# Kernel optimization log

Measured on AMD Instinct MI355X. Metric: run time of the kernel, lower is better.

## Reference

```python
import jax, jax.numpy as jnp
import numpy as np

C = 1024
H = 16
K = 2  # num_states
B, N = 4, 4096


def setup_inputs() -> dict:
    key = jax.random.key(0)
    ks_ = jax.random.split(key, 12)
    s = 1.0 / np.sqrt(C)
    inp = {
        "x": jax.random.normal(ks_[0], (B, N, C), dtype=jnp.float32),
        "Wq": jax.random.normal(ks_[1], (C, C), dtype=jnp.float32) * s,
        "bq": jnp.zeros((C,), dtype=jnp.float32),
        "Wk": jax.random.normal(ks_[2], (K, C, C), dtype=jnp.float32) * s,
        "bk": jnp.zeros((K, C), dtype=jnp.float32),
        "Wv": jax.random.normal(ks_[3], (K, C, C), dtype=jnp.float32) * s,
        "bv": jnp.zeros((K, C), dtype=jnp.float32),
        "Wo": jax.random.normal(ks_[4], (C, C), dtype=jnp.float32) * s,
        "bo": jnp.zeros((C,), dtype=jnp.float32),
        "ln_g": jnp.ones((C,), dtype=jnp.float32),
        "ln_b": jnp.zeros((C,), dtype=jnp.float32),
    }
    return inp


def _heads(t):
    # [..., n, (h d)] -> [..., h, n, d]
    shp = t.shape
    d = shp[-1] // H
    t = t.reshape(shp[:-1] + (H, d))
    return jnp.swapaxes(t, -2, -3)


def reference(x, Wq, bq, Wk, bk, Wv, bv, Wo, bo, ln_g, ln_b):
    dtype = x.dtype
    # residual single-layer projections (ResidualMLP with num_layers=-1)
    q = x + jnp.einsum('bnc,cd->bnd', x, Wq) + bq
    ks = x[None] + jnp.einsum('bnc,kcd->kbnd', x, Wk) + bk[:, None, None, :]
    vs = x[None] + jnp.einsum('bnc,kcd->kbnd', x, Wv) + bv[:, None, None, :]
    q = _heads(q)        # [b,h,n,d]
    ks = _heads(ks)      # [k,b,h,n,d]
    vs = _heads(vs)      # [k,b,h,n,d]
    scale = 1.0 / jnp.sqrt(jnp.asarray(N, dtype=jnp.float32))
    ks = ks.astype(jnp.float32) * scale
    vs = vs.astype(jnp.float32) * scale
    # per-state KV outer-products: [k,b,h,d,e]
    states = jnp.einsum('kbhnd,kbhne->kbhde', ks, vs)
    state = jnp.prod(states, axis=0)  # [b,h,d,e]
    out = jnp.einsum('bhnd,bhde->bhne', q.astype(jnp.float32), state)
    out = out.astype(dtype)
    # [b,h,n,d] -> [b,n,(h d)]
    out = jnp.swapaxes(out, 1, 2).reshape(x.shape[0], x.shape[1], C)
    # LayerNorm
    mu = jnp.mean(out, axis=-1, keepdims=True)
    var = jnp.var(out, axis=-1, keepdims=True)
    out = (out - mu) / jnp.sqrt(var + 1e-5) * ln_g + ln_b
    out = jnp.einsum('bnc,cd->bnd', out, Wo) + bo
    return out
```

## Files before the change

### kernel.cpp

```cpp
#include <hip/hip_runtime.h>
#include <hip/hip_bf16.h>

typedef __attribute__((ext_vector_type(8))) short bf16x8;
typedef __attribute__((ext_vector_type(4))) float f32x4;
typedef __attribute__((ext_vector_type(4))) short s16x4;

__device__ __forceinline__ short f2bf(float f) {
  union { float f; unsigned u; } v; v.f = f;
  unsigned r = v.u + 0x7fffu + ((v.u >> 16) & 1u);
  return (short)(r >> 16);
}

__device__ __forceinline__ float bf2f(short s) {
  union { float f; unsigned u; } v; v.u = ((unsigned)(unsigned short)s) << 16;
  return v.f;
}

#define GLD_LDS(g, l) __builtin_amdgcn_global_load_lds( \
    (const __attribute__((address_space(1))) void*)(g), \
    (__attribute__((address_space(3))) void*)(l), 16, 0, 0)

__global__ __launch_bounds__(256)
void convt_k(const float* __restrict__ x, short* __restrict__ xb,
             short* __restrict__ xbT) {
  __shared__ short tile[64][72];
  const int b = blockIdx.z;
  const int n0 = blockIdx.y * 64;
  const int c0 = blockIdx.x * 64;
  const int t = threadIdx.x;
  const int nl = t >> 4;
  const int c4 = (t & 15) << 2;
  const float* xp = x + ((size_t)b * 4096 + n0) * 1024 + c0;
#pragma unroll
  for (int i = 0; i < 4; ++i) {
    const int n = nl + 16 * i;
    const float4 v = *(const float4*)(xp + (size_t)n * 1024 + c4);
    s16x4 o;
    o[0] = f2bf(v.x); o[1] = f2bf(v.y); o[2] = f2bf(v.z); o[3] = f2bf(v.w);
    *(s16x4*)(&xb[((size_t)b * 4096 + n0 + n) * 1024 + c0 + c4]) = o;
    *(s16x4*)(&tile[n][c4]) = o;
  }
  __syncthreads();
  const int cll = t >> 4;
  const int n4 = (t & 15) << 2;
#pragma unroll
  for (int i = 0; i < 4; ++i) {
    const int c = cll + 16 * i;
    s16x4 o;
    o[0] = tile[n4 + 0][c]; o[1] = tile[n4 + 1][c];
    o[2] = tile[n4 + 2][c]; o[3] = tile[n4 + 3][c];
    *(s16x4*)(&xbT[((size_t)b * 1024 + c0 + c) * 4096 + n0 + n4]) = o;
  }
}

__global__ void twc_k(const float* __restrict__ Wq, const float* __restrict__ Wk,
                      const float* __restrict__ Wv, const float* __restrict__ Wo,
                      const float* __restrict__ lng, short* __restrict__ dst,
                      short* __restrict__ wqn) {
  __shared__ float tile[32][33];
  const int z = blockIdx.z;
  const float* src = (z == 0) ? Wq
                   : (z == 1) ? Wk
                   : (z == 2) ? (Wk + 1048576)
                   : (z == 3) ? Wv
                   : (z == 4) ? (Wv + 1048576)
                   : Wo;
  short* d = dst + (size_t)z * 1048576;
  const int tx = threadIdx.x, ty = threadIdx.y;
  const int c0 = blockIdx.y * 32, d0 = blockIdx.x * 32;
#pragma unroll
  for (int i = 0; i < 4; ++i) {
    const int cc = c0 + ty + i * 8;
    const float v = src[(size_t)cc * 1024 + d0 + tx];
    tile[ty + i * 8][tx] = v;
    if (z == 0)
      wqn[(size_t)cc * 1024 + d0 + tx] = f2bf(v + (cc == d0 + tx ? 1.0f : 0.0f));
  }
  __syncthreads();
#pragma unroll
  for (int i = 0; i < 4; ++i) {
    const int cc = c0 + tx;
    const int dd = d0 + ty + i * 8;
    float v = tile[tx][ty + i * 8];
    if (z < 5) {
      if (cc == dd) v += 1.0f;
    } else {
      v *= lng[cc];
    }
    d[(size_t)dd * 1024 + cc] = f2bf(v);
  }
}

__global__ __launch_bounds__(256)
void colsumT_k(const short* __restrict__ xbT, float* __restrict__ s) {
  const int row = blockIdx.x;
  const int tid = threadIdx.x;
  const short* p = xbT + ((size_t)row << 12);
  float acc = 0.f;
#pragma unroll
  for (int it = 0; it < 2; ++it) {
    const bf16x8 v = *(const bf16x8*)(p + ((tid + it * 256) << 3));
#pragma unroll
    for (int j = 0; j < 8; ++j) acc += bf2f(v[j]);
  }
#pragma unroll
  for (int o = 32; o > 0; o >>= 1) acc += __shfl_down(acc, o);
  __shared__ float red[4];
  if ((tid & 63) == 0) red[tid >> 6] = acc;
  __syncthreads();
  if (tid == 0) s[row] = red[0] + red[1] + red[2] + red[3];
}

__global__ __launch_bounds__(256)
void gemv_k(const short* __restrict__ wt, const float* __restrict__ s,
            float* __restrict__ u, float* __restrict__ w) {
  const int z = blockIdx.z, b = blockIdx.y;
  const int lane = threadIdx.x & 63, wid = threadIdx.x >> 6;
  const short* W = wt + ((size_t)(z + 1) << 20);
  const float* sb = s + b * 1024;
  float* outp = (z < 2) ? (u + (z * 4 + b) * 1024) : (w + ((z - 2) * 4 + b) * 1024);
#pragma unroll 1
  for (int it = 0; it < 16; ++it) {
    const int d = blockIdx.x * 64 + wid * 16 + it;
    const short* row = W + (size_t)d * 1024 + lane * 16;
    float acc = 0.f;
#pragma unroll
    for (int j = 0; j < 16; ++j) acc += bf2f(row[j]) * sb[lane * 16 + j];
#pragma unroll
    for (int o = 32; o > 0; o >>= 1) acc += __shfl_down(acc, o);
    if (lane == 0) outp[d] = acc;
  }
}

__global__ __launch_bounds__(256)
void ut_k(const float* __restrict__ Wo, const float* __restrict__ lng,
          const float* __restrict__ lnb, const float* __restrict__ bo,
          float* __restrict__ u, float* __restrict__ t) {
  const int dl = threadIdx.x & 63;
  const int dd = blockIdx.x * 64 + dl;
  const int part = threadIdx.x >> 6;
  float su = 0.f, st = 0.f;
  for (int c = part * 256; c < part * 256 + 256; ++c) {
    const float w = Wo[(size_t)c * 1024 + dd];
    su += lng[c] * w;
    st += lnb[c] * w;
  }
  __shared__ float rs[4][64], rt[4][64];
  rs[part][dl] = su; rt[part][dl] = st;
  __syncthreads();
  if (part == 0) {
    su = rs[0][dl] + rs[1][dl] + rs[2][dl] + rs[3][dl];
    st = rt[0][dl] + rt[1][dl] + rt[2][dl] + rt[3][dl];
    u[dd] = su;
    t[dd] = st + bo[dd];
  }
}

__global__ __launch_bounds__(512, 2)
void gram_k(const short* __restrict__ xbT, float* __restrict__ Pg) {
  extern __shared__ short lds[];
  const int tid = threadIdx.x;
  const int lane = tid & 63;
  const int wv = tid >> 6;
  const int wm = wv >> 2;
  const int wn = wv & 3;
  const int swz = ((blockIdx.x & 7) << 5) + (blockIdx.x >> 3);
  const int kz = swz & 3, tl = (swz >> 2) & 15, b = swz >> 6;
  const int bm0 = (tl >> 2) << 8, bn0 = (tl & 3) << 8;
  const int koff = kz << 10;
  const short* Ap = xbT + ((size_t)b << 22);
  float* po = Pg + ((size_t)((kz << 2) + b) << 20);

  const int lrow = ((lane >> 3) << 1) | ((lane >> 2) & 1);
  const int kc = ((lane & 3) ^ ((lane >> 3) & 3)) << 3;
  const int cl = lane & 15;
  const int khi = lane >> 4;

  f32x4 acc[8][4];
#pragma unroll
  for (int i = 0; i < 8; ++i)
#pragma unroll
    for (int j = 0; j < 4; ++j) acc[i][j] = f32x4{0.f, 0.f, 0.f, 0.f};

  auto stage = [&](int buf, int t) {
    const int k0 = koff + (t << 5) + kc;
    short* ab = lds + (buf << 14);
    short* bb = ab + 8192;
#pragma unroll
    for (int c = 0; c < 2; ++c) {
      const int un = wv * 2 + c;
      GLD_LDS(Ap + (size_t)(bm0 + (un << 4) + lrow) * 4096 + k0, ab + (un << 9));
      GLD_LDS(Ap + (size_t)(bn0 + (un << 4) + lrow) * 4096 + k0, bb + (un << 9));
    }
  };

  auto compute = [&](int buf) {
    const short* ab = lds + (buf << 14);
    const short* bb = ab + 8192;
    bf16x8 af[8], bfr[4];
#pragma unroll
    for (int i = 0; i < 8; ++i) {
      const int R = (wm << 7) + (i << 4) + cl;
      af[i] = *(const bf16x8*)(ab + (R << 5) + ((khi ^ ((R >> 1) & 3)) << 3));
    }
#pragma unroll
    for (int j = 0; j < 4; ++j) {
      const int C = (wn << 6) + (j << 4) + cl;
      bfr[j] = *(const bf16x8*)(bb + (C << 5) + ((khi ^ ((C >> 1) & 3)) << 3));
    }
#pragma unroll
    for (int i = 0; i < 8; ++i)
#pragma unroll
      for (int j = 0; j < 4; ++j)
        acc[i][j] = __builtin_amdgcn_mfma_f32_16x16x32_bf16(af[i], bfr[j], acc[i][j], 0, 0, 0);
  };

  stage(0, 0);
  stage(1, 1);
  asm volatile("s_waitcnt vmcnt(4)" ::: "memory");
  __builtin_amdgcn_s_barrier();
#pragma unroll 1
  for (int t = 0; t < 30; ++t) {
    stage((t + 2) & 3, t + 2);
    compute(t & 3);
    asm volatile("s_waitcnt vmcnt(4)" ::: "memory");
    __builtin_amdgcn_s_barrier();
  }
  compute(2);
  asm volatile("s_waitcnt vmcnt(0)" ::: "memory");
  __builtin_amdgcn_s_barrier();
  compute(3);

#pragma unroll
  for (int i = 0; i < 8; ++i)
#pragma unroll
    for (int j = 0; j < 4; ++j) {
      const int col = bn0 + (wn << 6) + (j << 4) + cl;
      const int rowb = bm0 + (wm << 7) + (i << 4) + (khi << 2);
#pragma unroll
      for (int r = 0; r < 4; ++r)
        po[(size_t)(rowb + r) * 1024 + col] = acc[i][j][r];
    }
}

__global__ __launch_bounds__(512, 2)
void oat_k(const short* __restrict__ xb, const short* __restrict__ Beff,
           const float* __restrict__ rq, short* __restrict__ oat,
           float* __restrict__ musum, float* __restrict__ sqsum) {
  extern __shared__ short lds[];
  const int tid = threadIdx.x;
  const int lane = tid & 63;
  const int wv = tid >> 6;
  const int wm = wv >> 2;
  const int wn = wv & 3;
  const int swz = ((blockIdx.x & 7) << 5) + (blockIdx.x >> 3);
  const int b = swz >> 6;
  const int tl = swz & 63;
  const int bm0 = (tl >> 2) << 8;
  const int bn0 = (tl & 3) << 8;
  const short* Ap = xb + ((size_t)b << 22);
  const short* Bp = Beff + ((size_t)b << 20);

  const int lrow = ((lane >> 3) << 1) | ((lane >> 2) & 1);
  const int kc = ((lane & 3) ^ ((lane >> 3) & 3)) << 3;
  const int cl = lane & 15;
  const int khi = lane >> 4;

  f32x4 acc[8][4];
#pragma unroll
  for (int i = 0; i < 8; ++i)
#pragma unroll
    for (int j = 0; j < 4; ++j) acc[i][j] = f32x4{0.f, 0.f, 0.f, 0.f};

  auto stage = [&](int buf, int t) {
    const int k0 = (t << 5) + kc;
    short* ab = lds + (buf << 14);
    short* bb = ab + 8192;
#pragma unroll
    for (int c = 0; c < 2; ++c) {
      const int un = wv * 2 + c;
      GLD_LDS(Ap + (size_t)(bm0 + (un << 4) + lrow) * 1024 + k0, ab + (un << 9));
      GLD_LDS(Bp + (size_t)(bn0 + (un << 4) + lrow) * 1024 + k0, bb + (un << 9));
    }
  };

  auto compute = [&](int buf) {
    const short* ab = lds + (buf << 14);
    const short* bb = ab + 8192;
    bf16x8 af[8], bfr[4];
#pragma unroll
    for (int i = 0; i < 8; ++i) {
      const int R = (wm << 7) + (i << 4) + cl;
      af[i] = *(const bf16x8*)(ab + (R << 5) + ((khi ^ ((R >> 1) & 3)) << 3));
    }
#pragma unroll
    for (int j = 0; j < 4; ++j) {
      const int C = (wn << 6) + (j << 4) + cl;
      bfr[j] = *(const bf16x8*)(bb + (C << 5) + ((khi ^ ((C >> 1) & 3)) << 3));
    }
#pragma unroll
    for (int i = 0; i < 8; ++i)
#pragma unroll
      for (int j = 0; j < 4; ++j)
        acc[i][j] = __builtin_amdgcn_mfma_f32_16x16x32_bf16(af[i], bfr[j], acc[i][j], 0, 0, 0);
  };

  stage(0, 0);
  stage(1, 1);
  asm volatile("s_waitcnt vmcnt(4)" ::: "memory");
  __builtin_amdgcn_s_barrier();
#pragma unroll 1
  for (int t = 0; t < 30; ++t) {
    stage((t + 2) & 3, t + 2);
    compute(t & 3);
    asm volatile("s_waitcnt vmcnt(4)" ::: "memory");
    __builtin_amdgcn_s_barrier();
  }
  compute(2);
  asm volatile("s_waitcnt vmcnt(0)" ::: "memory");
  __builtin_amdgcn_s_barrier();
  compute(3);

#pragma unroll
  for (int i = 0; i < 8; ++i) {
    const int rowb = bm0 + (wm << 7) + (i << 4) + (khi << 2);
    s16x4 pk[4];
#pragma unroll
    for (int j = 0; j < 4; ++j) {
      const int col = bn0 + (wn << 6) + (j << 4) + cl;
      const float rqc = rq[b * 1024 + col];
#pragma unroll
      for (int r = 0; r < 4; ++r) pk[j][r] = f2bf(acc[i][j][r] + rqc);
#pragma unroll
      for (int r = 0; r < 4; ++r)
        oat[(size_t)(b * 4096 + rowb + r) * 1024 + col] = pk[j][r];
    }
#pragma unroll
    for (int r = 0; r < 4; ++r) {
      float sv = 0.f, sq = 0.f;
#pragma unroll
      for (int j = 0; j < 4; ++j) {
        const float fv = bf2f(pk[j][r]);
        sv += fv; sq += fv * fv;
      }
#pragma unroll
      for (int m = 1; m < 16; m <<= 1) {
        sv += __shfl_xor(sv, m);
        sq += __shfl_xor(sq, m);
      }
      if (cl == 0) {
        atomicAdd(&musum[b * 4096 + rowb + r], sv);
        atomicAdd(&sqsum[b * 4096 + rowb + r], sq);
      }
    }
  }
}

__global__ __launch_bounds__(256)
void greduce_k(const float* __restrict__ Pg, short* __restrict__ G) {
  const int b = blockIdx.x >> 10;
  const int local = ((blockIdx.x & 1023) << 10) + (threadIdx.x << 2);
  float4 a = {0.f, 0.f, 0.f, 0.f};
#pragma unroll
  for (int kz = 0; kz < 4; ++kz) {
    const float4 v = *(const float4*)(Pg + (((size_t)((kz << 2) + b)) << 20) + local);
    a.x += v.x; a.y += v.y; a.z += v.z; a.w += v.w;
  }
  const float sc = 1.0f / 4096.0f;
  s16x4 o;
  o[0] = f2bf(a.x * sc); o[1] = f2bf(a.y * sc);
  o[2] = f2bf(a.z * sc); o[3] = f2bf(a.w * sc);
  *(s16x4*)(G + ((size_t)b << 20) + local) = o;
}

__global__ __launch_bounds__(256)
void gemm128_k(const short* __restrict__ A, const short* __restrict__ Bt,
               short* __restrict__ out) {
  __shared__ short Ab[2][4096];
  __shared__ short Bb[2][4096];
  const int bid = blockIdx.x;
  const int swz = ((bid & 7) << 4) + (bid >> 3);
  const int bm0 = (swz >> 3) << 7;
  const int bn0 = (swz & 7) << 7;
  const short* Bp = Bt + ((size_t)blockIdx.y << 20);
  short* op = out + ((size_t)blockIdx.y << 21);
  const int tid = threadIdx.x, lane = tid & 63, wid = tid >> 6;
  const int wm = (wid >> 1) << 6, wn = (wid & 1) << 6;
  const int lrow = ((lane >> 3) << 1) | ((lane >> 2) & 1);
  const int kc = ((lane & 3) ^ ((lane >> 3) & 3)) << 3;
  const int cl = lane & 15, khi = lane >> 4;

  f32x4 acc[4][4];
#pragma unroll
  for (int i = 0; i < 4; ++i)
#pragma unroll
    for (int j = 0; j < 4; ++j) acc[i][j] = f32x4{0.f, 0.f, 0.f, 0.f};

  auto stage = [&](int buf, int t) {
    const int k0 = (t << 5) + kc;
#pragma unroll
    for (int c = 0; c < 2; ++c) {
      const int un = wid * 2 + c;
      GLD_LDS(A + (size_t)(bm0 + (un << 4) + lrow) * 1024 + k0, &Ab[buf][un << 9]);
      GLD_LDS(Bp + (size_t)(bn0 + (un << 4) + lrow) * 1024 + k0, &Bb[buf][un << 9]);
    }
  };

  stage(0, 0);
  __syncthreads();
#pragma unroll 1
  for (int t = 0; t < 32; ++t) {
    const int cur = t & 1;
    if (t < 31) stage(cur ^ 1, t + 1);
    const short* ab = Ab[cur];
    const short* bb = Bb[cur];
    bf16x8 af[4], bfr[4];
#pragma unroll
    for (int i = 0; i < 4; ++i) {
      const int R = wm + (i << 4) + cl;
      af[i] = *(const bf16x8*)(ab + (R << 5) + ((khi ^ ((R >> 1) & 3)) << 3));
    }
#pragma unroll
    for (int j = 0; j < 4; ++j) {
      const int C = wn + (j << 4) + cl;
      bfr[j] = *(const bf16x8*)(bb + (C << 5) + ((khi ^ ((C >> 1) & 3)) << 3));
    }
#pragma unroll
    for (int i = 0; i < 4; ++i)
#pragma unroll
      for (int j = 0; j < 4; ++j)
        acc[i][j] = __builtin_amdgcn_mfma_f32_16x16x32_bf16(af[i], bfr[j], acc[i][j], 0, 0, 0);
    __syncthreads();
  }

#pragma unroll
  for (int i = 0; i < 4; ++i)
#pragma unroll
    for (int j = 0; j < 4; ++j) {
      const int col = bn0 + wn + (j << 4) + cl;
      const int rowb = bm0 + wm + (i << 4) + (khi << 2);
#pragma unroll
      for (int r = 0; r < 4; ++r)
        op[(size_t)(rowb + r) * 1024 + col] = f2bf(acc[i][j][r]);
    }
}

__global__ __launch_bounds__(256)
void states2_k(const short* __restrict__ wt, const short* __restrict__ Tt,
               float* __restrict__ M) {
  __shared__ short Al[64 * 40];
  __shared__ short Bl[64 * 40];
  const int h = blockIdx.x, b = blockIdx.y, k = blockIdx.z;
  const short* Ap = wt + ((size_t)(1 + k) << 20) + ((size_t)(h * 64) << 10);
  const short* Bp = Tt + ((size_t)b << 21) + ((size_t)(k * 1024 + h * 64) << 10);
  const int tid = threadIdx.x, lane = tid & 63, wid = tid >> 6;
  const int srow = tid >> 2, sch = (tid & 3) << 3;

  f32x4 acc[4];
#pragma unroll
  for (int j = 0; j < 4; ++j) acc[j] = f32x4{0.f, 0.f, 0.f, 0.f};

#pragma unroll 1
  for (int ns = 0; ns < 1024; ns += 32) {
    bf16x8 va = *(const bf16x8*)(Ap + ((size_t)srow << 10) + ns + sch);
    bf16x8 vb = *(const bf16x8*)(Bp + ((size_t)srow << 10) + ns + sch);
    __syncthreads();
    *(bf16x8*)(Al + srow * 40 + sch) = va;
    *(bf16x8*)(Bl + srow * 40 + sch) = vb;
    __syncthreads();
    bf16x8 a = *(const bf16x8*)(Al + (wid * 16 + (lane & 15)) * 40 + ((lane >> 4) << 3));
#pragma unroll
    for (int j = 0; j < 4; ++j) {
      bf16x8 bb = *(const bf16x8*)(Bl + (j * 16 + (lane & 15)) * 40 + ((lane >> 4) << 3));
      acc[j] = __builtin_amdgcn_mfma_f32_16x16x32_bf16(a, bb, acc[j], 0, 0, 0);
    }
  }
  const size_t mb = ((size_t)((k * 4 + b) * 16 + h)) << 12;
  const int r0 = wid * 16 + ((lane >> 4) << 2);
  const int cl = lane & 15;
#pragma unroll
  for (int j = 0; j < 4; ++j)
#pragma unroll
    for (int r = 0; r < 4; ++r)
      M[mb + (size_t)(r0 + r) * 64 + j * 16 + cl] = acc[j][r];
}

__global__ __launch_bounds__(256)
void combine_k(const float* __restrict__ M, const float* __restrict__ u,
               const float* __restrict__ w, const float* __restrict__ bk,
               const float* __restrict__ bv, short* __restrict__ stt) {
  const int bh = blockIdx.x;
  const int b = bh >> 4, h = bh & 15;
  const float invN = 1.0f / 4096.0f;
  for (int t = threadIdx.x; t < 4096; t += 256) {
    const int d = t >> 6, e = t & 63;
    float m[2];
#pragma unroll
    for (int k = 0; k < 2; ++k) {
      const float bkd = bk[k * 1024 + h * 64 + d];
      const float bve = bv[k * 1024 + h * 64 + e];
      const float ud = u[(k * 4 + b) * 1024 + h * 64 + d];
      const float we = w[(k * 4 + b) * 1024 + h * 64 + e];
      m[k] = M[(((size_t)((k * 4 + b) * 16 + h)) << 12) + t]
           + (ud * bve + bkd * we + 4096.f * bkd * bve) * invN;
    }
    stt[(bh << 12) + (e << 6) + d] = f2bf(m[0] * m[1]);
  }
}

__global__ __launch_bounds__(256)
void weff_k(const short* __restrict__ stt, const short* __restrict__ wqn,
            const float* __restrict__ bq, short* __restrict__ Beff,
            float* __restrict__ rq) {
  __shared__ short S[64][72];
  const int bh = blockIdx.x;
  const int b = bh >> 4, h = bh & 15;
  const int tid = threadIdx.x, lane = tid & 63, wid = tid >> 6;
  {
    const int r = tid >> 2, c8 = (tid & 3) << 4;
    *(bf16x8*)(&S[r][c8]) = *(const bf16x8*)(stt + (bh << 12) + (r << 6) + c8);
    *(bf16x8*)(&S[r][c8 + 8]) = *(const bf16x8*)(stt + (bh << 12) + (r << 6) + c8 + 8);
  }
  __syncthreads();
  if (wid == 0) {
    float acc = 0.f;
#pragma unroll 1
    for (int d = 0; d < 64; ++d) acc += bq[h * 64 + d] * bf2f(S[lane][d]);
    rq[b * 1024 + h * 64 + lane] = acc;
  }
  const int cl = lane & 15, khi = lane >> 4;
  bf16x8 af[4][2];
#pragma unroll
  for (int mi = 0; mi < 4; ++mi)
#pragma unroll
    for (int kk = 0; kk < 2; ++kk)
      af[mi][kk] = *(const bf16x8*)(&S[mi * 16 + cl][kk * 32 + khi * 8]);
  const short* wq = wqn + h * 64;
  short* bdst = Beff + ((size_t)b << 20) + ((size_t)(h * 64) << 10);
#pragma unroll 1
  for (int nf = 0; nf < 16; ++nf) {
    const int c0 = wid * 256 + nf * 16;
    const bf16x8 bf0 = *(const bf16x8*)(wq + (size_t)(c0 + cl) * 1024 + khi * 8);
    const bf16x8 bf1 = *(const bf16x8*)(wq + (size_t)(c0 + cl) * 1024 + 32 + khi * 8);
    f32x4 a4[4];
#pragma unroll
    for (int mi = 0; mi < 4; ++mi) {
      a4[mi] = f32x4{0.f, 0.f, 0.f, 0.f};
      a4[mi] = __builtin_amdgcn_mfma_f32_16x16x32_bf16(af[mi][0], bf0, a4[mi], 0, 0, 0);
      a4[mi] = __builtin_amdgcn_mfma_f32_16x16x32_bf16(af[mi][1], bf1, a4[mi], 0, 0, 0);
    }
#pragma unroll
    for (int mi = 0; mi < 4; ++mi)
#pragma unroll
      for (int r = 0; r < 4; ++r)
        bdst[(size_t)(mi * 16 + khi * 4 + r) * 1024 + c0 + cl] = f2bf(a4[mi][r]);
  }
}

__global__ __launch_bounds__(512, 2)
void gemmo_k(const short* __restrict__ A, const short* __restrict__ WT,
             const float* __restrict__ musum, const float* __restrict__ sqsum,
             const float* __restrict__ uu, const float* __restrict__ tt,
             float* __restrict__ fout) {
  extern __shared__ short lds[];
  const int tid = threadIdx.x;
  const int lane = tid & 63;
  const int wv = tid >> 6;
  const int wm = wv >> 2;
  const int wn = wv & 3;
  const int swz = ((blockIdx.x & 7) << 5) + (blockIdx.x >> 3);
  const int bm0 = (swz & 63) << 8;
  const int bn0 = (swz >> 6) << 8;

  const int lrow = ((lane >> 3) << 1) | ((lane >> 2) & 1);
  const int kc = ((lane & 3) ^ ((lane >> 3) & 3)) << 3;
  const int cl = lane & 15;
  const int khi = lane >> 4;

  f32x4 acc[8][4];
#pragma unroll
  for (int i = 0; i < 8; ++i)
#pragma unroll
    for (int j = 0; j < 4; ++j) acc[i][j] = f32x4{0.f, 0.f, 0.f, 0.f};

  auto stage = [&](int buf, int t) {
    const int k0 = (t << 5) + kc;
    short* ab = lds + (buf << 14);
    short* bb = ab + 8192;
#pragma unroll
    for (int c = 0; c < 2; ++c) {
      const int un = wv * 2 + c;
      GLD_LDS(A + (size_t)(bm0 + (un << 4) + lrow) * 1024 + k0, ab + (un << 9));
      GLD_LDS(WT + (size_t)(bn0 + (un << 4) + lrow) * 1024 + k0, bb + (un << 9));
    }
  };

  auto compute = [&](int buf) {
    const short* ab = lds + (buf << 14);
    const short* bb = ab + 8192;
    bf16x8 af[8], bfr[4];
#pragma unroll
    for (int i = 0; i < 8; ++i) {
      const int R = (wm << 7) + (i << 4) + cl;
      af[i] = *(const bf16x8*)(ab + (R << 5) + ((khi ^ ((R >> 1) & 3)) << 3));
    }
#pragma unroll
    for (int j = 0; j < 4; ++j) {
      const int C = (wn << 6) + (j << 4) + cl;
      bfr[j] = *(const bf16x8*)(bb + (C << 5) + ((khi ^ ((C >> 1) & 3)) << 3));
    }
#pragma unroll
    for (int i = 0; i < 8; ++i)
#pragma unroll
      for (int j = 0; j < 4; ++j)
        acc[i][j] = __builtin_amdgcn_mfma_f32_16x16x32_bf16(af[i], bfr[j], acc[i][j], 0, 0, 0);
  };

  stage(0, 0);
  stage(1, 1);
  asm volatile("s_waitcnt vmcnt(4)" ::: "memory");
  __builtin_amdgcn_s_barrier();
#pragma unroll 1
  for (int t = 0; t < 30; ++t) {
    stage((t + 2) & 3, t + 2);
    compute(t & 3);
    asm volatile("s_waitcnt vmcnt(4)" ::: "memory");
    __builtin_amdgcn_s_barrier();
  }
  compute(2);
  asm volatile("s_waitcnt vmcnt(0)" ::: "memory");
  __builtin_amdgcn_s_barrier();
  compute(3);

#pragma unroll
  for (int i = 0; i < 8; ++i) {
    const int rowb = bm0 + (wm << 7) + (i << 4) + (khi << 2);
    const float4 ms = *(const float4*)(musum + rowb);
    const float4 qs = *(const float4*)(sqsum + rowb);
    float mu[4], rs[4];
    mu[0] = ms.x * (1.0f / 1024.0f); mu[1] = ms.y * (1.0f / 1024.0f);
    mu[2] = ms.z * (1.0f / 1024.0f); mu[3] = ms.w * (1.0f / 1024.0f);
    rs[0] = rsqrtf(fmaxf(qs.x * (1.0f / 1024.0f) - mu[0] * mu[0], 0.f) + 1e-5f);
    rs[1] = rsqrtf(fmaxf(qs.y * (1.0f / 1024.0f) - mu[1] * mu[1], 0.f) + 1e-5f);
    rs[2] = rsqrtf(fmaxf(qs.z * (1.0f / 1024.0f) - mu[2] * mu[2], 0.f) + 1e-5f);
    rs[3] = rsqrtf(fmaxf(qs.w * (1.0f / 1024.0f) - mu[3] * mu[3], 0.f) + 1e-5f);
#pragma unroll
    for (int j = 0; j < 4; ++j) {
      const int col = bn0 + (wn << 6) + (j << 4) + cl;
      const float uc = uu[col];
      const float tc = tt[col];
#pragma unroll
      for (int r = 0; r < 4; ++r)
        fout[(size_t)(rowb + r) * 1024 + col] = rs[r] * (acc[i][j][r] - mu[r] * uc) + tc;
    }
  }
}

extern "C" void kernel_launch(void* const* d_in, const int* in_sizes, int n_in,
                              void* d_out, int out_size, void* d_ws, size_t ws_size,
                              hipStream_t stream) {
  const float* x = (const float*)d_in[0];
  const float* Wq = (const float*)d_in[1];
  const float* bq = (const float*)d_in[2];
  const float* Wk = (const float*)d_in[3];
  const float* bk = (const float*)d_in[4];
  const float* Wv = (const float*)d_in[5];
  const float* bv = (const float*)d_in[6];
  const float* Wo = (const float*)d_in[7];
  const float* bo = (const float*)d_in[8];
  const float* lng = (const float*)d_in[9];
  const float* lnb = (const float*)d_in[10];

  char* ws = (char*)d_ws;
  short* xb = (short*)(ws + 0);
  short* wt = (short*)(ws + 33554432);
  short* wqn = (short*)(ws + 46137344);
  short* Beff = (short*)(ws + 48234496);
  float* rq = (float*)(ws + 56623104);
  float* musum = (float*)(ws + 56639488);
  float* sqsum = (float*)(ws + 56705024);
  float* s = (float*)(ws + 56770560);
  float* u = (float*)(ws + 56786944);
  float* w = (float*)(ws + 56819712);
  float* uu = (float*)(ws + 56852480);
  float* tt = (float*)(ws + 56856576);
  short* xbT = (short*)(ws + 79691776);
  short* Gt = (short*)(ws + 113246208);
  short* Tt = (short*)(ws + 121634816);
  float* M = (float*)(ws + 138412032);
  short* stt = (short*)(ws + 142606336);
  float* Pg = (float*)(ws + 143351808);
  short* oat = xbT;

  hipMemsetAsync(musum, 0, 131072, stream);
  convt_k<<<dim3(16, 64, 4), 256, 0, stream>>>(x, xb, xbT);
  twc_k<<<dim3(32, 32, 6), dim3(32, 8), 0, stream>>>(Wq, Wk, Wv, Wo, lng, wt, wqn);
  colsumT_k<<<4096, 256, 0, stream>>>(xbT, s);
  gemv_k<<<dim3(16, 4, 4), 256, 0, stream>>>(wt, s, u, w);
  ut_k<<<16, 256, 0, stream>>>(Wo, lng, lnb, bo, uu, tt);

  gram_k<<<256, 512, 131072, stream>>>(xbT, Pg);
  greduce_k<<<4096, 256, 0, stream>>>(Pg, Gt);
  gemm128_k<<<dim3(128, 4), 256, 0, stream>>>(wt + 3145728, Gt, Tt);
  states2_k<<<dim3(16, 4, 2), 256, 0, stream>>>(wt, Tt, M);
  combine_k<<<64, 256, 0, stream>>>(M, u, w, bk, bv, stt);
  weff_k<<<64, 256, 0, stream>>>(stt, wqn, bq, Beff, rq);

  oat_k<<<256, 512, 131072, stream>>>(xb, Beff, rq, oat, musum, sqsum);
  gemmo_k<<<256, 512, 131072, stream>>>(oat, wt + 5242880, musum, sqsum, uu, tt,
                                        (float*)d_out);
}
```

Before: 283.8 us.

## Fuse column sums and small state kernels, deepen gemm128 pipeline, remap block swizzles

Folds the column-sum reduction into the conversion/transpose kernel using atomics, which removes colsumT_k and one pass over xbT. states2, combine and weff are merged into a single kernel so the M and stt intermediates are never written to memory. gemm128 moves to a 4-buffer dynamic-LDS pipeline with a prefetch distance of two and explicit waitcnt/barrier calls. The block-index swizzles in gram_k and gemmo_k are remapped to improve L2 locality. The fused state kernel launches only 64 blocks while each runs both k-loops serially, so it may lose parallelism.

```diff
diff --git a/kernel.cpp b/kernel.cpp
--- a/kernel.cpp
+++ b/kernel.cpp
@@ -22,8 +22,9 @@
 
 __global__ __launch_bounds__(256)
 void convt_k(const float* __restrict__ x, short* __restrict__ xb,
-             short* __restrict__ xbT) {
+             short* __restrict__ xbT, float* __restrict__ s) {
   __shared__ short tile[64][72];
+  __shared__ float red[4][64];
   const int b = blockIdx.z;
   const int n0 = blockIdx.y * 64;
   const int c0 = blockIdx.x * 64;
@@ -51,6 +52,15 @@
     o[2] = tile[n4 + 2][c]; o[3] = tile[n4 + 3][c];
     *(s16x4*)(&xbT[((size_t)b * 1024 + c0 + c) * 4096 + n0 + n4]) = o;
   }
+  const int part = t >> 6, col = t & 63;
+  float cs = 0.f;
+#pragma unroll
+  for (int i = 0; i < 16; ++i) cs += bf2f(tile[part * 16 + i][col]);
+  red[part][col] = cs;
+  __syncthreads();
+  if (part == 0)
+    atomicAdd(&s[b * 1024 + c0 + col],
+              red[0][col] + red[1][col] + red[2][col] + red[3][col]);
 }
 
 __global__ void twc_k(const float* __restrict__ Wq, const float* __restrict__ Wk,
@@ -92,26 +102,6 @@
 }
 
 __global__ __launch_bounds__(256)
-void colsumT_k(const short* __restrict__ xbT, float* __restrict__ s) {
-  const int row = blockIdx.x;
-  const int tid = threadIdx.x;
-  const short* p = xbT + ((size_t)row << 12);
-  float acc = 0.f;
-#pragma unroll
-  for (int it = 0; it < 2; ++it) {
-    const bf16x8 v = *(const bf16x8*)(p + ((tid + it * 256) << 3));
-#pragma unroll
-    for (int j = 0; j < 8; ++j) acc += bf2f(v[j]);
-  }
-#pragma unroll
-  for (int o = 32; o > 0; o >>= 1) acc += __shfl_down(acc, o);
-  __shared__ float red[4];
-  if ((tid & 63) == 0) red[tid >> 6] = acc;
-  __syncthreads();
-  if (tid == 0) s[row] = red[0] + red[1] + red[2] + red[3];
-}
-
-__global__ __launch_bounds__(256)
 void gemv_k(const short* __restrict__ wt, const float* __restrict__ s,
             float* __restrict__ u, float* __restrict__ w) {
   const int z = blockIdx.z, b = blockIdx.y;
@@ -165,7 +155,9 @@
   const int wm = wv >> 2;
   const int wn = wv & 3;
   const int swz = ((blockIdx.x & 7) << 5) + (blockIdx.x >> 3);
-  const int kz = swz & 3, tl = (swz >> 2) & 15, b = swz >> 6;
+  const int b = swz >> 6;
+  const int kz = (swz >> 4) & 3;
+  const int tl = swz & 15;
   const int bm0 = (tl >> 2) << 8, bn0 = (tl & 3) << 8;
   const int koff = kz << 10;
   const short* Ap = xbT + ((size_t)b << 22);
@@ -373,11 +365,10 @@
   *(s16x4*)(G + ((size_t)b << 20) + local) = o;
 }
 
-__global__ __launch_bounds__(256)
+__global__ __launch_bounds__(256, 2)
 void gemm128_k(const short* __restrict__ A, const short* __restrict__ Bt,
                short* __restrict__ out) {
-  __shared__ short Ab[2][4096];
-  __shared__ short Bb[2][4096];
+  extern __shared__ short lds[];
   const int bid = blockIdx.x;
   const int swz = ((bid & 7) << 4) + (bid >> 3);
   const int bm0 = (swz >> 3) << 7;
@@ -398,22 +389,19 @@
 
   auto stage = [&](int buf, int t) {
     const int k0 = (t << 5) + kc;
+    short* ab = lds + (buf << 13);
+    short* bb = ab + 4096;
 #pragma unroll
     for (int c = 0; c < 2; ++c) {
       const int un = wid * 2 + c;
-      GLD_LDS(A + (size_t)(bm0 + (un << 4) + lrow) * 1024 + k0, &Ab[buf][un << 9]);
-      GLD_LDS(Bp + (size_t)(bn0 + (un << 4) + lrow) * 1024 + k0, &Bb[buf][un << 9]);
-    }
-  };
-
-  stage(0, 0);
-  __syncthreads();
-#pragma unroll 1
-  for (int t = 0; t < 32; ++t) {
-    const int cur = t & 1;
-    if (t < 31) stage(cur ^ 1, t + 1);
-    const short* ab = Ab[cur];
-    const short* bb = Bb[cur];
+      GLD_LDS(A + (size_t)(bm0 + (un << 4) + lrow) * 1024 + k0, ab + (un << 9));
+      GLD_LDS(Bp + (size_t)(bn0 + (un << 4) + lrow) * 1024 + k0, bb + (un << 9));
+    }
+  };
+
+  auto compute = [&](int buf) {
+    const short* ab = lds + (buf << 13);
+    const short* bb = ab + 4096;
     bf16x8 af[4], bfr[4];
 #pragma unroll
     for (int i = 0; i < 4; ++i) {
@@ -430,8 +418,23 @@
 #pragma unroll
       for (int j = 0; j < 4; ++j)
         acc[i][j] = __builtin_amdgcn_mfma_f32_16x16x32_bf16(af[i], bfr[j], acc[i][j], 0, 0, 0);
-    __syncthreads();
-  }
+  };
+
+  stage(0, 0);
+  stage(1, 1);
+  asm volatile("s_waitcnt vmcnt(4)" ::: "memory");
+  __builtin_amdgcn_s_barrier();
+#pragma unroll 1
+  for (int t = 0; t < 30; ++t) {
+    stage((t + 2) & 3, t + 2);
+    compute(t & 3);
+    asm volatile("s_waitcnt vmcnt(4)" ::: "memory");
+    __builtin_amdgcn_s_barrier();
+  }
+  compute(2);
+  asm volatile("s_waitcnt vmcnt(0)" ::: "memory");
+  __builtin_amdgcn_s_barrier();
+  compute(3);
 
 #pragma unroll
   for (int i = 0; i < 4; ++i)
@@ -446,89 +449,76 @@
 }
 
 __global__ __launch_bounds__(256)
-void states2_k(const short* __restrict__ wt, const short* __restrict__ Tt,
-               float* __restrict__ M) {
+void sw_k(const short* __restrict__ wt, const short* __restrict__ Tt,
+          const float* __restrict__ u, const float* __restrict__ w,
+          const float* __restrict__ bk, const float* __restrict__ bv,
+          const short* __restrict__ wqn, const float* __restrict__ bq,
+          short* __restrict__ Beff, float* __restrict__ rq) {
   __shared__ short Al[64 * 40];
   __shared__ short Bl[64 * 40];
-  const int h = blockIdx.x, b = blockIdx.y, k = blockIdx.z;
-  const short* Ap = wt + ((size_t)(1 + k) << 20) + ((size_t)(h * 64) << 10);
-  const short* Bp = Tt + ((size_t)b << 21) + ((size_t)(k * 1024 + h * 64) << 10);
+  __shared__ short S[64][72];
+  const int h = blockIdx.x & 15, b = blockIdx.x >> 4;
   const int tid = threadIdx.x, lane = tid & 63, wid = tid >> 6;
   const int srow = tid >> 2, sch = (tid & 3) << 3;
-
-  f32x4 acc[4];
-#pragma unroll
-  for (int j = 0; j < 4; ++j) acc[j] = f32x4{0.f, 0.f, 0.f, 0.f};
-
-#pragma unroll 1
-  for (int ns = 0; ns < 1024; ns += 32) {
-    bf16x8 va = *(const bf16x8*)(Ap + ((size_t)srow << 10) + ns + sch);
-    bf16x8 vb = *(const bf16x8*)(Bp + ((size_t)srow << 10) + ns + sch);
-    __syncthreads();
-    *(bf16x8*)(Al + srow * 40 + sch) = va;
-    *(bf16x8*)(Bl + srow * 40 + sch) = vb;
-    __syncthreads();
-    bf16x8 a = *(const bf16x8*)(Al + (wid * 16 + (lane & 15)) * 40 + ((lane >> 4) << 3));
-#pragma unroll
-    for (int j = 0; j < 4; ++j) {
-      bf16x8 bb = *(const bf16x8*)(Bl + (j * 16 + (lane & 15)) * 40 + ((lane >> 4) << 3));
-      acc[j] = __builtin_amdgcn_mfma_f32_16x16x32_bf16(a, bb, acc[j], 0, 0, 0);
-    }
-  }
-  const size_t mb = ((size_t)((k * 4 + b) * 16 + h)) << 12;
-  const int r0 = wid * 16 + ((lane >> 4) << 2);
-  const int cl = lane & 15;
-#pragma unroll
-  for (int j = 0; j < 4; ++j)
-#pragma unroll
-    for (int r = 0; r < 4; ++r)
-      M[mb + (size_t)(r0 + r) * 64 + j * 16 + cl] = acc[j][r];
-}
-
-__global__ __launch_bounds__(256)
-void combine_k(const float* __restrict__ M, const float* __restrict__ u,
-               const float* __restrict__ w, const float* __restrict__ bk,
-               const float* __restrict__ bv, short* __restrict__ stt) {
-  const int bh = blockIdx.x;
-  const int b = bh >> 4, h = bh & 15;
+  const int cl = lane & 15, khi = lane >> 4;
+
+  f32x4 acc2[2][4];
+#pragma unroll
+  for (int k = 0; k < 2; ++k)
+#pragma unroll
+    for (int j = 0; j < 4; ++j) acc2[k][j] = f32x4{0.f, 0.f, 0.f, 0.f};
+
+#pragma unroll
+  for (int k = 0; k < 2; ++k) {
+    const short* Ap = wt + ((size_t)(1 + k) << 20) + ((size_t)(h * 64) << 10);
+    const short* Bp = Tt + ((size_t)b << 21) + ((size_t)(k * 1024 + h * 64) << 10);
+#pragma unroll 1
+    for (int ns = 0; ns < 1024; ns += 32) {
+      bf16x8 va = *(const bf16x8*)(Ap + ((size_t)srow << 10) + ns + sch);
+      bf16x8 vb = *(const bf16x8*)(Bp + ((size_t)srow << 10) + ns + sch);
+      __syncthreads();
+      *(bf16x8*)(Al + srow * 40 + sch) = va;
+      *(bf16x8*)(Bl + srow * 40 + sch) = vb;
+      __syncthreads();
+      bf16x8 a = *(const bf16x8*)(Al + (wid * 16 + cl) * 40 + (khi << 3));
+#pragma unroll
+      for (int j = 0; j < 4; ++j) {
+        bf16x8 bb = *(const bf16x8*)(Bl + (j * 16 + cl) * 40 + (khi << 3));
+        acc2[k][j] = __builtin_amdgcn_mfma_f32_16x16x32_bf16(a, bb, acc2[k][j], 0, 0, 0);
+      }
+    }
+  }
+
+  const int d0 = wid * 16 + (khi << 2);
   const float invN = 1.0f / 4096.0f;
-  for (int t = threadIdx.x; t < 4096; t += 256) {
-    const int d = t >> 6, e = t & 63;
-    float m[2];
-#pragma unroll
-    for (int k = 0; k < 2; ++k) {
-      const float bkd = bk[k * 1024 + h * 64 + d];
-      const float bve = bv[k * 1024 + h * 64 + e];
-      const float ud = u[(k * 4 + b) * 1024 + h * 64 + d];
-      const float we = w[(k * 4 + b) * 1024 + h * 64 + e];
-      m[k] = M[(((size_t)((k * 4 + b) * 16 + h)) << 12) + t]
-           + (ud * bve + bkd * we + 4096.f * bkd * bve) * invN;
-    }
-    stt[(bh << 12) + (e << 6) + d] = f2bf(m[0] * m[1]);
-  }
-}
-
-__global__ __launch_bounds__(256)
-void weff_k(const short* __restrict__ stt, const short* __restrict__ wqn,
-            const float* __restrict__ bq, short* __restrict__ Beff,
-            float* __restrict__ rq) {
-  __shared__ short S[64][72];
-  const int bh = blockIdx.x;
-  const int b = bh >> 4, h = bh & 15;
-  const int tid = threadIdx.x, lane = tid & 63, wid = tid >> 6;
-  {
-    const int r = tid >> 2, c8 = (tid & 3) << 4;
-    *(bf16x8*)(&S[r][c8]) = *(const bf16x8*)(stt + (bh << 12) + (r << 6) + c8);
-    *(bf16x8*)(&S[r][c8 + 8]) = *(const bf16x8*)(stt + (bh << 12) + (r << 6) + c8 + 8);
+#pragma unroll
+  for (int j = 0; j < 4; ++j) {
+    const int e = j * 16 + cl;
+    s16x4 pk;
+#pragma unroll
+    for (int r = 0; r < 4; ++r) {
+      const int d = d0 + r;
+      float m[2];
+#pragma unroll
+      for (int k = 0; k < 2; ++k) {
+        const float bkd = bk[k * 1024 + h * 64 + d];
+        const float bve = bv[k * 1024 + h * 64 + e];
+        const float ud = u[(k * 4 + b) * 1024 + h * 64 + d];
+        const float we = w[(k * 4 + b) * 1024 + h * 64 + e];
+        m[k] = acc2[k][j][r] + (ud * bve + bkd * we + 4096.f * bkd * bve) * invN;
+      }
+      pk[r] = f2bf(m[0] * m[1]);
+    }
+    *(s16x4*)(&S[e][d0]) = pk;
   }
   __syncthreads();
+
   if (wid == 0) {
     float acc = 0.f;
 #pragma unroll 1
     for (int d = 0; d < 64; ++d) acc += bq[h * 64 + d] * bf2f(S[lane][d]);
     rq[b * 1024 + h * 64 + lane] = acc;
   }
-  const int cl = lane & 15, khi = lane >> 4;
   bf16x8 af[4][2];
 #pragma unroll
   for (int mi = 0; mi < 4; ++mi)
@@ -569,8 +559,8 @@
   const int wm = wv >> 2;
   const int wn = wv & 3;
   const int swz = ((blockIdx.x & 7) << 5) + (blockIdx.x >> 3);
-  const int bm0 = (swz & 63) << 8;
-  const int bn0 = (swz >> 6) << 8;
+  const int bm0 = (swz >> 2) << 8;
+  const int bn0 = (swz & 3) << 8;
 
   const int lrow = ((lane >> 3) << 1) | ((lane >> 2) & 1);
   const int kc = ((lane & 3) ^ ((lane >> 3) & 3)) << 3;
@@ -687,24 +677,19 @@
   short* xbT = (short*)(ws + 79691776);
   short* Gt = (short*)(ws + 113246208);
   short* Tt = (short*)(ws + 121634816);
-  float* M = (float*)(ws + 138412032);
-  short* stt = (short*)(ws + 142606336);
   float* Pg = (float*)(ws + 143351808);
   short* oat = xbT;
 
-  hipMemsetAsync(musum, 0, 131072, stream);
-  convt_k<<<dim3(16, 64, 4), 256, 0, stream>>>(x, xb, xbT);
+  hipMemsetAsync(musum, 0, 147456, stream);
+  convt_k<<<dim3(16, 64, 4), 256, 0, stream>>>(x, xb, xbT, s);
   twc_k<<<dim3(32, 32, 6), dim3(32, 8), 0, stream>>>(Wq, Wk, Wv, Wo, lng, wt, wqn);
-  colsumT_k<<<4096, 256, 0, stream>>>(xbT, s);
   gemv_k<<<dim3(16, 4, 4), 256, 0, stream>>>(wt, s, u, w);
   ut_k<<<16, 256, 0, stream>>>(Wo, lng, lnb, bo, uu, tt);
 
   gram_k<<<256, 512, 131072, stream>>>(xbT, Pg);
   greduce_k<<<4096, 256, 0, stream>>>(Pg, Gt);
-  gemm128_k<<<dim3(128, 4), 256, 0, stream>>>(wt + 3145728, Gt, Tt);
-  states2_k<<<dim3(16, 4, 2), 256, 0, stream>>>(wt, Tt, M);
-  combine_k<<<64, 256, 0, stream>>>(M, u, w, bk, bv, stt);
-  weff_k<<<64, 256, 0, stream>>>(stt, wqn, bq, Beff, rq);
+  gemm128_k<<<dim3(128, 4), 256, 65536, stream>>>(wt + 3145728, Gt, Tt);
+  sw_k<<<64, 256, 0, stream>>>(wt, Tt, u, w, bk, bv, wqn, bq, Beff, rq);
 
   oat_k<<<256, 512, 131072, stream>>>(xb, Beff, rq, oat, musum, sqsum);
   gemmo_k<<<256, 512, 131072, stream>>>(oat, wt + 5242880, musum, sqsum, uu, tt,
```

New measurement: 271.6 us. -4.3%, faster.
